# Kernel optimization log

Hardware: AMD Instinct MI355X
Metric: run time of the kernel (lower is better)

The kernel has to match this reference:

```python
import jax, jax.numpy as jnp
import numpy as np

BS, N, H = 8, 64, 512
L = 5
HH, WW = 14, 14


def setup_inputs() -> dict:
    key = jax.random.key(0)
    ks = jax.random.split(key, 6)
    roi_feature_single = jax.random.normal(ks[0], (BS, N, H), dtype=jnp.float32)
    img_featmap = jax.random.normal(ks[1], (BS, H, HH, WW), dtype=jnp.float32)
    # torch init: weight ~ N(0, 0.01), bias = 0
    node_W = jax.random.normal(ks[2], (L, H, H), dtype=jnp.float32) * 0.01
    node_b = jnp.zeros((L, H), dtype=jnp.float32)
    edge_W = jax.random.normal(ks[3], (L, H, H), dtype=jnp.float32) * 0.01
    edge_b = jnp.zeros((L, H), dtype=jnp.float32)
    full_mask = jax.random.randint(ks[4], (BS, N, N), 0, 2, dtype=jnp.int32)
    return {
        "roi_feature_single": roi_feature_single,
        "img_featmap": img_featmap,
        "node_W": node_W,
        "node_b": node_b,
        "edge_W": edge_W,
        "edge_b": edge_b,
        "full_mask": full_mask,
    }


def reference(roi_feature_single, img_featmap, node_W, node_b, edge_W, edge_b, full_mask):
    # mask: [bs, N, N, 1], float
    mask = full_mask.astype(jnp.float32)[..., None]
    denom = jnp.sum(mask, axis=-2) + 1.0  # [bs, N, 1]

    # AdaptiveAvgPool2d((1,1)) on N*N repeats of img_featmap == global mean over (H, W)
    edge_init = jnp.mean(img_featmap, axis=(2, 3))  # [bs, hidden]
    edge_state = jnp.broadcast_to(edge_init[:, None, None, :], (BS, N, N, H))

    node_state = roi_feature_single  # [bs, N, hidden]

    for t in range(L):
        nm = jnp.einsum('bnh,oh->bno', node_state, node_W[t]) + node_b[t]          # node_fc
        em = jnp.einsum('bijh,oh->bijo', edge_state, edge_W[t]) + edge_b[t]        # edge_fc
        col = nm[:, None, :, :]                      # feature_col_large [bs,1,N,h]
        edge_feat = nm[:, :, None, :] + col + em     # row + col + edge messages
        edge_state = jax.nn.leaky_relu(edge_feat)    # negative_slope=0.01 (torch default)
        agg = jnp.sum(edge_state * col * mask, axis=-2)   # masked sum over j -> [bs,N,h]
        node_feat = (nm + agg) / denom
        node_state = node_state + jax.nn.leaky_relu(node_feat)

    roi_col = jnp.broadcast_to(node_state[:, :, None, :], (BS, N, N, H))
    roi_row = jnp.broadcast_to(node_state[:, None, :, :], (BS, N, N, H))
    return jnp.concatenate([roi_col, roi_row], axis=-1)  # [bs, N, N, 2*hidden]
```

## Files before the change

### kernel.cpp

```cpp
#include <hip/hip_runtime.h>
#include <hip/hip_bf16.h>

#define BS 8
#define NN 64
#define HD 512
#define NLAYER 5

typedef short bf16x8 __attribute__((ext_vector_type(8)));
typedef float f32x4 __attribute__((ext_vector_type(4)));

__device__ __forceinline__ float lrelu(float x) { return x > 0.f ? x : 0.01f * x; }

__device__ __forceinline__ void cp16(const void* g, void* l) {
    __builtin_amdgcn_global_load_lds(
        (const __attribute__((address_space(1))) unsigned int*)g,
        (__attribute__((address_space(3))) unsigned int*)l,
        16, 0, 0);
}

__global__ __launch_bounds__(256) void prep_kernel(
    const float* __restrict__ roi, const float* __restrict__ img,
    const float* __restrict__ nW, const float* __restrict__ eW,
    const int* __restrict__ mask,
    __hip_bfloat16* __restrict__ nWb, __hip_bfloat16* __restrict__ eWb,
    float* __restrict__ nodef, __hip_bfloat16* __restrict__ nodeb,
    float* __restrict__ edge_init, float* __restrict__ denom)
{
    int bid = blockIdx.x, tid = threadIdx.x;
    if (bid < 2560) {
        const float* src = (bid < 1280) ? nW : eW;
        __hip_bfloat16* dst = (bid < 1280) ? nWb : eWb;
        int base = ((bid < 1280) ? bid : bid - 1280) * 1024 + tid * 4;
#pragma unroll
        for (int k = 0; k < 4; ++k) dst[base + k] = __float2bfloat16(src[base + k]);
    } else if (bid < 2816) {
        int base = (bid - 2560) * 1024 + tid * 4;
#pragma unroll
        for (int k = 0; k < 4; ++k) {
            float v = roi[base + k];
            nodef[base + k] = v;
            nodeb[base + k] = __float2bfloat16(v);
        }
    } else if (bid < 3840) {
        int pid = (bid - 2816) * 4 + (tid >> 6);
        int l = tid & 63;
        const float* p = img + (size_t)pid * 196;
        float s = 0.f;
        for (int x = l; x < 196; x += 64) s += p[x];
#pragma unroll
        for (int off = 1; off < 64; off <<= 1) s += __shfl_xor(s, off, 64);
        if (l == 0) edge_init[pid] = s * (1.f / 196.f);
    } else {
        int pid = (bid - 3840) * 256 + tid;
        if (pid < 512) {
            const int* m = mask + pid * 64;
            int s = 0;
#pragma unroll
            for (int j = 0; j < 64; ++j) s += m[j];
            denom[pid] = (float)s + 1.f;
        }
    }
}

__global__ __launch_bounds__(256) void em0_kernel(
    const float* __restrict__ edge_init,
    const float* __restrict__ eW0,
    const float* __restrict__ eB0,
    float* __restrict__ em0)
{
    int W = blockIdx.x * 4 + (threadIdx.x >> 6);
    int l = threadIdx.x & 63;
    int b = W >> 9, o = W & 511;
    const float4* ei = (const float4*)(edge_init + b * 512);
    const float4* w4 = (const float4*)(eW0 + (size_t)o * 512);
    float4 a0 = ei[l * 2], a1 = ei[l * 2 + 1];
    float4 b0 = w4[l * 2], b1 = w4[l * 2 + 1];
    float s = a0.x * b0.x + a0.y * b0.y + a0.z * b0.z + a0.w * b0.w
            + a1.x * b1.x + a1.y * b1.y + a1.z * b1.z + a1.w * b1.w;
#pragma unroll
    for (int off = 1; off < 64; off <<= 1) s += __shfl_xor(s, off, 64);
    if (l == 0) em0[W] = s + eB0[o];
}

__global__ __launch_bounds__(256, 4) void nm_gemm(
    const __hip_bfloat16* __restrict__ A,
    const __hip_bfloat16* __restrict__ W,
    const float* __restrict__ bias,
    float* __restrict__ nm)
{
    __shared__ __align__(16) __hip_bfloat16 sA[32 * 64];
    __shared__ __align__(16) __hip_bfloat16 sB[64 * 64];
    int tid = threadIdx.x;
    int bm = blockIdx.x, bn = blockIdx.y;
    int w = tid >> 6, l = tid & 63;
    int wm = w & 1, wn = w >> 1;
    int lq = l >> 4, lr = l & 15;

    const char* aBase = (const char*)A + (size_t)bm * 32 * 1024;
    const char* bBase = (const char*)W + (size_t)bn * 64 * 1024;
    int rowA = tid >> 3;
    int gA = rowA * 1024 + (((tid & 7) ^ (rowA & 7)) << 4);
    int lO = tid * 16;
    int sw = lr & 7;

    f32x4 acc[2] = {};

    for (int kt = 0; kt < 8; ++kt) {
        int ko = kt * 128;
        cp16(aBase + gA + ko, (char*)sA + lO);
        cp16(bBase + gA + ko, (char*)sB + lO);
        cp16(bBase + gA + 32768 + ko, (char*)sB + lO + 4096);
        __syncthreads();
#pragma unroll
        for (int kk = 0; kk < 2; ++kk) {
            bf16x8 af = *(const bf16x8*)&sA[(wm * 16 + lr) * 64 + (((kk * 4 + lq) ^ sw) << 3)];
#pragma unroll
            for (int ni = 0; ni < 2; ++ni) {
                bf16x8 bv = *(const bf16x8*)&sB[(wn * 32 + ni * 16 + lr) * 64 + (((kk * 4 + lq) ^ sw) << 3)];
                acc[ni] = __builtin_amdgcn_mfma_f32_16x16x32_bf16(af, bv, acc[ni], 0, 0, 0);
            }
        }
        __syncthreads();
    }
#pragma unroll
    for (int ni = 0; ni < 2; ++ni) {
        int col = bn * 64 + wn * 32 + ni * 16 + lr;
        float bv = bias[col];
#pragma unroll
        for (int r = 0; r < 4; ++r) {
            int row = bm * 32 + wm * 16 + lq * 4 + r;
            nm[(size_t)row * 512 + col] = acc[ni][r] + bv;
        }
    }
}

__global__ __launch_bounds__(256) void edge_rank1(
    const float* __restrict__ nm, const float* __restrict__ em0,
    const int* __restrict__ mask,
    __hip_bfloat16* __restrict__ es_dst,
    const float* __restrict__ denom,
    float* __restrict__ nodef, __hip_bfloat16* __restrict__ nodeb)
{
    int g = blockIdx.x >> 1, ch = blockIdx.x & 1;
    int c = ch * 256 + threadIdx.x;
    int b = g >> 6;
    float nmi = nm[(size_t)g * 512 + c];
    float emb = em0[b * 512 + c];
    const float* nmb = nm + (size_t)b * 64 * 512;
    const int* mrow = mask + g * 64;
    __hip_bfloat16* erow = es_dst + (size_t)g * 64 * 512 + c;
    float aggv = 0.f;
#pragma unroll 4
    for (int j = 0; j < 64; ++j) {
        float nmj = nmb[j * 512 + c];
        float es = lrelu(nmi + nmj + emb);
        erow[(size_t)j * 512] = __float2bfloat16(es);
        aggv += es * nmj * (float)mrow[j];
    }
    float nf = (nmi + aggv) / denom[g];
    size_t idx = (size_t)g * 512 + c;
    float ns = nodef[idx] + lrelu(nf);
    nodef[idx] = ns;
    nodeb[idx] = __float2bfloat16(ns);
}

__global__ __launch_bounds__(256, 6) void edge_fused(
    const __hip_bfloat16* __restrict__ es_src,
    const __hip_bfloat16* __restrict__ eW,
    const float* __restrict__ eB,
    const float* __restrict__ nm,
    const int* __restrict__ mask,
    __hip_bfloat16* __restrict__ es_dst,
    const float* __restrict__ denom,
    float* __restrict__ nodef, __hip_bfloat16* __restrict__ nodeb,
    int write_es)
{
    __shared__ __align__(16) __hip_bfloat16 sA[64 * 64];
    __shared__ __align__(16) __hip_bfloat16 sB[64 * 64];
    int tid = threadIdx.x;
    int bm = blockIdx.x;
    int bn = blockIdx.y;
    int w = tid >> 6, l = tid & 63;
    int lq = l >> 4, lr = l & 15;

    const char* aBase = (const char*)es_src + (size_t)bm * 64 * 1024;
    const char* bBase = (const char*)eW + (size_t)bn * 64 * 1024;
    int rrow = tid >> 3;
    int gOff = rrow * 1024 + ((((tid & 7) ^ (rrow & 7))) << 4);
    int lOff = tid * 16;
    int sw = lr & 7;

    f32x4 acc[4] = {};

    for (int kt = 0; kt < 8; ++kt) {
        int ko = kt * 128;
        cp16(aBase + gOff + ko,         (char*)sA + lOff);
        cp16(aBase + gOff + 32768 + ko, (char*)sA + lOff + 4096);
        cp16(bBase + gOff + ko,         (char*)sB + lOff);
        cp16(bBase + gOff + 32768 + ko, (char*)sB + lOff + 4096);
        __syncthreads();
#pragma unroll
        for (int kk = 0; kk < 2; ++kk) {
            bf16x8 bf = *(const bf16x8*)&sB[(w * 16 + lr) * 64 + (((kk * 4 + lq) ^ sw) << 3)];
#pragma unroll
            for (int mi = 0; mi < 4; ++mi) {
                bf16x8 af = *(const bf16x8*)&sA[(mi * 16 + lr) * 64 + (((kk * 4 + lq) ^ sw) << 3)];
                acc[mi] = __builtin_amdgcn_mfma_f32_16x16x32_bf16(af, bf, acc[mi], 0, 0, 0);
            }
        }
        __syncthreads();
    }

    int g = bm;
    int b = g >> 6;
    int c = bn * 64 + w * 16 + lr;

    float nmraw = nm[(size_t)g * 512 + c];
    float nmi = nmraw + eB[c];
    const float* nmb = nm + (size_t)b * 64 * 512;
    const int* mrow = mask + g * 64;
    float aggv = 0.f;

#pragma unroll
    for (int mi = 0; mi < 4; ++mi) {
#pragma unroll
        for (int r = 0; r < 4; ++r) {
            int j = mi * 16 + lq * 4 + r;
            float mf = (float)mrow[j];
            float nmj = nmb[(size_t)j * 512 + c];
            float es = lrelu(acc[mi][r] + nmi + nmj);
            if (write_es) es_dst[((size_t)(g * 64 + j)) * 512 + c] = __float2bfloat16(es);
            aggv += es * nmj * mf;
        }
    }
    aggv += __shfl_xor(aggv, 16, 64);
    aggv += __shfl_xor(aggv, 32, 64);
    if (lq == 0) {
        size_t oidx = (size_t)g * 512 + c;
        float nf = (nmraw + aggv) / denom[g];
        float ns = nodef[oidx] + lrelu(nf);
        nodef[oidx] = ns;
        nodeb[oidx] = __float2bfloat16(ns);
    }
}

__global__ __launch_bounds__(256) void out_kernel(
    const float* __restrict__ nodef, float* __restrict__ out)
{
    size_t ch = (size_t)blockIdx.x * 256 + threadIdx.x;
    int c4 = (int)(ch & 255);
    size_t r = ch >> 8;
    int b = (int)(r >> 12);
    int i = (int)((r >> 6) & 63);
    int j = (int)(r & 63);
    int c = c4 * 4;
    const float* src = (c < 512) ? (nodef + ((size_t)(b * 64 + i)) * 512 + c)
                                 : (nodef + ((size_t)(b * 64 + j)) * 512 + (c - 512));
    *reinterpret_cast<float4*>(out + ch * 4) = *reinterpret_cast<const float4*>(src);
}

extern "C" void kernel_launch(void* const* d_in, const int* in_sizes, int n_in,
                              void* d_out, int out_size, void* d_ws, size_t ws_size,
                              hipStream_t stream) {
    const float* roi  = (const float*)d_in[0];
    const float* img  = (const float*)d_in[1];
    const float* nW   = (const float*)d_in[2];
    const float* nB   = (const float*)d_in[3];
    const float* eW   = (const float*)d_in[4];
    const float* eB   = (const float*)d_in[5];
    const int*   mask = (const int*)d_in[6];

    char* ob = (char*)d_out;
    const size_t ES_BYTES = (size_t)32768 * 512 * 2;
    __hip_bfloat16* es0   = (__hip_bfloat16*)(ob);
    __hip_bfloat16* es1   = (__hip_bfloat16*)(ob + ES_BYTES);
    __hip_bfloat16* eWb   = (__hip_bfloat16*)(ob + 2 * ES_BYTES);
    __hip_bfloat16* nWb   = (__hip_bfloat16*)(ob + 2 * ES_BYTES + 2621440);
    __hip_bfloat16* nodeb = (__hip_bfloat16*)(ob + 2 * ES_BYTES + 5242880);
    float*          nm    = (float*)(ob + 2 * ES_BYTES + 5767168);
    float*       edge_init= (float*)(ob + 2 * ES_BYTES + 6815744);
    float*          em0   = (float*)(ob + 2 * ES_BYTES + 6832128);

    char* ws = (char*)d_ws;
    float* nodef = (float*)(ws);
    float* denom = (float*)(ws + 1048576);
    float* outp  = (float*)d_out;

    prep_kernel<<<3842, 256, 0, stream>>>(roi, img, nW, eW, mask,
                                          nWb, eWb, nodef, nodeb, edge_init, denom);
    em0_kernel<<<1024, 256, 0, stream>>>(edge_init, eW, eB, em0);

    nm_gemm<<<dim3(16, 8), 256, 0, stream>>>(nodeb, nWb, nB, nm);
    edge_rank1<<<1024, 256, 0, stream>>>(nm, em0, mask, es0, denom, nodef, nodeb);

    for (int t = 1; t < NLAYER; ++t) {
        const __hip_bfloat16* src = (t & 1) ? es0 : es1;
        __hip_bfloat16* dst       = (t & 1) ? es1 : es0;
        nm_gemm<<<dim3(16, 8), 256, 0, stream>>>(nodeb, nWb + (size_t)t * 262144,
                                                 nB + t * 512, nm);
        edge_fused<<<dim3(512, 8), 256, 0, stream>>>(src, eWb + (size_t)t * 262144,
                                                     eB + t * 512, nm, mask,
                                                     dst, denom, nodef, nodeb,
                                                     (t < 4) ? 1 : 0);
    }

    out_kernel<<<32768, 256, 0, stream>>>(nodef, outp);
}
```

Before: 361.1 us.

## Split K across two warp groups in edge GEMM with LDS reduction

The edge_fused block grows from 256 to 512 threads. Two 256-thread groups each handle half of the K dimension, using separate LDS buffers, and then combine their partial accumulators through a shared-memory reduction before the epilogue. The goal is to halve the serial K loop per block and add latency hiding per CU. The cost is more LDS per block (about 32KB) and an extra reduction and barrier, which may reduce occupancy. The second group exits early, so the epilogue runs on half the threads.

```diff
diff --git a/kernel.cpp b/kernel.cpp
--- a/kernel.cpp
+++ b/kernel.cpp
@@ -164,7 +164,7 @@
     nodeb[idx] = __float2bfloat16(ns);
 }
 
-__global__ __launch_bounds__(256, 6) void edge_fused(
+__global__ __launch_bounds__(512, 6) void edge_fused(
     const __hip_bfloat16* __restrict__ es_src,
     const __hip_bfloat16* __restrict__ eW,
     const float* __restrict__ eB,
@@ -175,45 +175,69 @@
     float* __restrict__ nodef, __hip_bfloat16* __restrict__ nodeb,
     int write_es)
 {
-    __shared__ __align__(16) __hip_bfloat16 sA[64 * 64];
-    __shared__ __align__(16) __hip_bfloat16 sB[64 * 64];
+    __shared__ __align__(16) __hip_bfloat16 sA[2][64 * 64];
+    __shared__ __align__(16) __hip_bfloat16 sB[2][64 * 64];
+    __shared__ __align__(16) f32x4 sRed[1024];
     int tid = threadIdx.x;
     int bm = blockIdx.x;
     int bn = blockIdx.y;
-    int w = tid >> 6, l = tid & 63;
+    int grp = tid >> 8;
+    int t = tid & 255;
+    int l = tid & 63;
+    int wc = (tid >> 6) & 3;
     int lq = l >> 4, lr = l & 15;
 
     const char* aBase = (const char*)es_src + (size_t)bm * 64 * 1024;
     const char* bBase = (const char*)eW + (size_t)bn * 64 * 1024;
-    int rrow = tid >> 3;
-    int gOff = rrow * 1024 + ((((tid & 7) ^ (rrow & 7))) << 4);
-    int lOff = tid * 16;
+    int rrow = t >> 3;
+    int gOff = rrow * 1024 + ((((t & 7) ^ (rrow & 7))) << 4);
+    int lOff = t * 16;
     int sw = lr & 7;
+    int kbase = grp * 512;
+
+    char* sAg = (char*)sA[grp];
+    char* sBg = (char*)sB[grp];
 
     f32x4 acc[4] = {};
 
-    for (int kt = 0; kt < 8; ++kt) {
-        int ko = kt * 128;
-        cp16(aBase + gOff + ko,         (char*)sA + lOff);
-        cp16(aBase + gOff + 32768 + ko, (char*)sA + lOff + 4096);
-        cp16(bBase + gOff + ko,         (char*)sB + lOff);
-        cp16(bBase + gOff + 32768 + ko, (char*)sB + lOff + 4096);
+    for (int s = 0; s < 4; ++s) {
+        int ko = kbase + s * 128;
+        cp16(aBase + gOff + ko,         sAg + lOff);
+        cp16(aBase + gOff + 32768 + ko, sAg + lOff + 4096);
+        cp16(bBase + gOff + ko,         sBg + lOff);
+        cp16(bBase + gOff + 32768 + ko, sBg + lOff + 4096);
         __syncthreads();
+        const __hip_bfloat16* sAr = (const __hip_bfloat16*)sAg;
+        const __hip_bfloat16* sBr = (const __hip_bfloat16*)sBg;
 #pragma unroll
         for (int kk = 0; kk < 2; ++kk) {
-            bf16x8 bf = *(const bf16x8*)&sB[(w * 16 + lr) * 64 + (((kk * 4 + lq) ^ sw) << 3)];
+            bf16x8 bf = *(const bf16x8*)&sBr[(wc * 16 + lr) * 64 + (((kk * 4 + lq) ^ sw) << 3)];
 #pragma unroll
             for (int mi = 0; mi < 4; ++mi) {
-                bf16x8 af = *(const bf16x8*)&sA[(mi * 16 + lr) * 64 + (((kk * 4 + lq) ^ sw) << 3)];
+                bf16x8 af = *(const bf16x8*)&sAr[(mi * 16 + lr) * 64 + (((kk * 4 + lq) ^ sw) << 3)];
                 acc[mi] = __builtin_amdgcn_mfma_f32_16x16x32_bf16(af, bf, acc[mi], 0, 0, 0);
             }
         }
         __syncthreads();
     }
 
+    if (grp == 1) {
+#pragma unroll
+        for (int mi = 0; mi < 4; ++mi) sRed[t * 4 + mi] = acc[mi];
+    }
+    __syncthreads();
+    if (grp == 1) return;
+
+#pragma unroll
+    for (int mi = 0; mi < 4; ++mi) {
+        f32x4 o = sRed[t * 4 + mi];
+#pragma unroll
+        for (int r = 0; r < 4; ++r) acc[mi][r] += o[r];
+    }
+
     int g = bm;
     int b = g >> 6;
-    int c = bn * 64 + w * 16 + lr;
+    int c = bn * 64 + wc * 16 + lr;
 
     float nmraw = nm[(size_t)g * 512 + c];
     float nmi = nmraw + eB[c];
@@ -298,7 +322,7 @@
         __hip_bfloat16* dst       = (t & 1) ? es1 : es0;
         nm_gemm<<<dim3(16, 8), 256, 0, stream>>>(nodeb, nWb + (size_t)t * 262144,
                                                  nB + t * 512, nm);
-        edge_fused<<<dim3(512, 8), 256, 0, stream>>>(src, eWb + (size_t)t * 262144,
+        edge_fused<<<dim3(512, 8), 512, 0, stream>>>(src, eWb + (size_t)t * 262144,
                                                      eB + t * 512, nm, mask,
                                                      dst, denom, nodef, nodeb,
                                                      (t < 4) ? 1 : 0);
```

Result: slower. 473.9 us (+31.2%).

## Fuse node-message GEMM into edge kernel and stage edge-state stores through LDS

Applied to the files above, without the earlier changes.

Drops the separate nm_gemm launch for layers 1-4. Each edge_fused block now recomputes its 64x64 tile of node messages (this batch's nodes times a 64-column slice of the node weight) into LDS, and node-state bf16 buffers are ping-ponged so in-place updates do not race with other blocks' reads. Edge-state outputs are written first to a swizzled LDS tile and then copied to global memory as 16-byte vector stores, replacing scattered 2-byte strided writes. The cost is redundant node-GEMM work (each batch's tile is recomputed by 64 blocks), extra LDS use, and occupancy lowered from 6 to 5.

```diff
diff --git a/kernel.cpp b/kernel.cpp
--- a/kernel.cpp
+++ b/kernel.cpp
@@ -164,34 +164,70 @@
     nodeb[idx] = __float2bfloat16(ns);
 }
 
-__global__ __launch_bounds__(256, 6) void edge_fused(
+__global__ __launch_bounds__(256, 5) void edge_fused(
     const __hip_bfloat16* __restrict__ es_src,
     const __hip_bfloat16* __restrict__ eW,
     const float* __restrict__ eB,
-    const float* __restrict__ nm,
+    const __hip_bfloat16* __restrict__ ndb,
+    const __hip_bfloat16* __restrict__ nW,
+    const float* __restrict__ nB,
     const int* __restrict__ mask,
     __hip_bfloat16* __restrict__ es_dst,
     const float* __restrict__ denom,
-    float* __restrict__ nodef, __hip_bfloat16* __restrict__ nodeb,
+    float* __restrict__ nodef,
+    __hip_bfloat16* __restrict__ nodeb_out,
     int write_es)
 {
     __shared__ __align__(16) __hip_bfloat16 sA[64 * 64];
     __shared__ __align__(16) __hip_bfloat16 sB[64 * 64];
+    __shared__ __align__(16) float nmLDS[64 * 64];
     int tid = threadIdx.x;
-    int bm = blockIdx.x;
+    int g = blockIdx.x;
     int bn = blockIdx.y;
     int w = tid >> 6, l = tid & 63;
     int lq = l >> 4, lr = l & 15;
-
-    const char* aBase = (const char*)es_src + (size_t)bm * 64 * 1024;
-    const char* bBase = (const char*)eW + (size_t)bn * 64 * 1024;
+    int b = g >> 6;
+    int cl = w * 16 + lr;
+    int c  = bn * 64 + cl;
+
+    const char* aBase  = (const char*)es_src + (size_t)g * 65536;
+    const char* bBase  = (const char*)eW + (size_t)bn * 65536;
+    const char* naBase = (const char*)ndb + (size_t)b * 65536;
+    const char* nbBase = (const char*)nW + (size_t)bn * 65536;
     int rrow = tid >> 3;
     int gOff = rrow * 1024 + ((((tid & 7) ^ (rrow & 7))) << 4);
     int lOff = tid * 16;
     int sw = lr & 7;
 
+    f32x4 anm[4] = {};
+    for (int kt = 0; kt < 8; ++kt) {
+        int ko = kt * 128;
+        cp16(naBase + gOff + ko,         (char*)sA + lOff);
+        cp16(naBase + gOff + 32768 + ko, (char*)sA + lOff + 4096);
+        cp16(nbBase + gOff + ko,         (char*)sB + lOff);
+        cp16(nbBase + gOff + 32768 + ko, (char*)sB + lOff + 4096);
+        __syncthreads();
+#pragma unroll
+        for (int kk = 0; kk < 2; ++kk) {
+            bf16x8 bf = *(const bf16x8*)&sB[(w * 16 + lr) * 64 + (((kk * 4 + lq) ^ sw) << 3)];
+#pragma unroll
+            for (int mi = 0; mi < 4; ++mi) {
+                bf16x8 af = *(const bf16x8*)&sA[(mi * 16 + lr) * 64 + (((kk * 4 + lq) ^ sw) << 3)];
+                anm[mi] = __builtin_amdgcn_mfma_f32_16x16x32_bf16(af, bf, anm[mi], 0, 0, 0);
+            }
+        }
+        __syncthreads();
+    }
+
+    float nBc = nB[c];
+#pragma unroll
+    for (int mi = 0; mi < 4; ++mi)
+#pragma unroll
+        for (int r = 0; r < 4; ++r)
+            nmLDS[(mi * 16 + lq * 4 + r) * 64 + cl] = anm[mi][r] + nBc;
+    __syncthreads();
+
     f32x4 acc[4] = {};
-
     for (int kt = 0; kt < 8; ++kt) {
         int ko = kt * 128;
         cp16(aBase + gOff + ko,         (char*)sA + lOff);
@@ -211,14 +247,10 @@
         __syncthreads();
     }
 
-    int g = bm;
-    int b = g >> 6;
-    int c = bn * 64 + w * 16 + lr;
-
-    float nmraw = nm[(size_t)g * 512 + c];
+    float nmraw = nmLDS[(g & 63) * 64 + cl];
     float nmi = nmraw + eB[c];
-    const float* nmb = nm + (size_t)b * 64 * 512;
     const int* mrow = mask + g * 64;
+    char* esL = (char*)sA;
     float aggv = 0.f;
 
 #pragma unroll
@@ -227,9 +259,11 @@
         for (int r = 0; r < 4; ++r) {
             int j = mi * 16 + lq * 4 + r;
             float mf = (float)mrow[j];
-            float nmj = nmb[(size_t)j * 512 + c];
+            float nmj = nmLDS[j * 64 + cl];
             float es = lrelu(acc[mi][r] + nmi + nmj);
-            if (write_es) es_dst[((size_t)(g * 64 + j)) * 512 + c] = __float2bfloat16(es);
+            if (write_es)
+                *(__hip_bfloat16*)(esL + j * 128 + ((cl * 2) ^ ((j & 7) << 4))) =
+                    __float2bfloat16(es);
             aggv += es * nmj * mf;
         }
     }
@@ -240,7 +274,18 @@
         float nf = (nmraw + aggv) / denom[g];
         float ns = nodef[oidx] + lrelu(nf);
         nodef[oidx] = ns;
-        nodeb[oidx] = __float2bfloat16(ns);
+        nodeb_out[oidx] = __float2bfloat16(ns);
+    }
+    if (write_es) {
+        __syncthreads();
+        char* dst = (char*)es_dst + (size_t)g * 65536 + bn * 128;
+#pragma unroll
+        for (int s = 0; s < 2; ++s) {
+            int chunk = tid + s * 256;
+            int row = chunk >> 3, c16 = chunk & 7;
+            *(bf16x8*)(dst + (size_t)row * 1024 + c16 * 16) =
+                *(const bf16x8*)(esL + row * 128 + ((c16 * 16) ^ ((row & 7) << 4)));
+        }
     }
 }
 
@@ -276,10 +321,11 @@
     __hip_bfloat16* es1   = (__hip_bfloat16*)(ob + ES_BYTES);
     __hip_bfloat16* eWb   = (__hip_bfloat16*)(ob + 2 * ES_BYTES);
     __hip_bfloat16* nWb   = (__hip_bfloat16*)(ob + 2 * ES_BYTES + 2621440);
-    __hip_bfloat16* nodeb = (__hip_bfloat16*)(ob + 2 * ES_BYTES + 5242880);
-    float*          nm    = (float*)(ob + 2 * ES_BYTES + 5767168);
-    float*       edge_init= (float*)(ob + 2 * ES_BYTES + 6815744);
-    float*          em0   = (float*)(ob + 2 * ES_BYTES + 6832128);
+    __hip_bfloat16* ndb0  = (__hip_bfloat16*)(ob + 2 * ES_BYTES + 5242880);
+    __hip_bfloat16* ndb1  = (__hip_bfloat16*)(ob + 2 * ES_BYTES + 5767168);
+    float*          nm    = (float*)(ob + 2 * ES_BYTES + 6291456);
+    float*       edge_init= (float*)(ob + 2 * ES_BYTES + 7340032);
+    float*          em0   = (float*)(ob + 2 * ES_BYTES + 7356416);
 
     char* ws = (char*)d_ws;
     float* nodef = (float*)(ws);
@@ -287,20 +333,22 @@
     float* outp  = (float*)d_out;
 
     prep_kernel<<<3842, 256, 0, stream>>>(roi, img, nW, eW, mask,
-                                          nWb, eWb, nodef, nodeb, edge_init, denom);
+                                          nWb, eWb, nodef, ndb0, edge_init, denom);
     em0_kernel<<<1024, 256, 0, stream>>>(edge_init, eW, eB, em0);
 
-    nm_gemm<<<dim3(16, 8), 256, 0, stream>>>(nodeb, nWb, nB, nm);
-    edge_rank1<<<1024, 256, 0, stream>>>(nm, em0, mask, es0, denom, nodef, nodeb);
+    nm_gemm<<<dim3(16, 8), 256, 0, stream>>>(ndb0, nWb, nB, nm);
+    edge_rank1<<<1024, 256, 0, stream>>>(nm, em0, mask, es0, denom, nodef, ndb1);
 
     for (int t = 1; t < NLAYER; ++t) {
         const __hip_bfloat16* src = (t & 1) ? es0 : es1;
         __hip_bfloat16* dst       = (t & 1) ? es1 : es0;
-        nm_gemm<<<dim3(16, 8), 256, 0, stream>>>(nodeb, nWb + (size_t)t * 262144,
-                                                 nB + t * 512, nm);
+        const __hip_bfloat16* nin = (t & 1) ? ndb1 : ndb0;
+        __hip_bfloat16* nout      = (t & 1) ? ndb0 : ndb1;
         edge_fused<<<dim3(512, 8), 256, 0, stream>>>(src, eWb + (size_t)t * 262144,
-                                                     eB + t * 512, nm, mask,
-                                                     dst, denom, nodef, nodeb,
+                                                     eB + t * 512,
+                                                     nin, nWb + (size_t)t * 262144,
+                                                     nB + t * 512, mask,
+                                                     dst, denom, nodef, nout,
                                                      (t < 4) ? 1 : 0);
     }
 
```

Measured after the change: 430.3 us. +19.1%, slower.
